# Kernel optimization log

Hardware: AMD Instinct MI355X
Metric: run time of the kernel (lower is better)

## Reference

```python
import jax, jax.numpy as jnp
import numpy as np

K = 1.0            # curvature (manifold.k); sqrt(K)=1 simplifies formulas
EPS = 1e-5         # module eps used in variance rescale
MIN_NORM = 1e-8    # clamp for sqrt of Lorentz inners
MAX_EUCLID = 10.0  # rescale_to_max_euclid cap (keeps cosh/sinh in fp32 range)


def l_inner(x, y):
    # Lorentz inner product <x,y>_L = -x0*y0 + <x_s, y_s>, keepdim
    return -x[..., :1] * y[..., :1] + jnp.sum(x[..., 1:] * y[..., 1:], axis=-1, keepdims=True)


def centroid(x):
    # Lorentzian centroid over the group axis (dim=-2)
    avg = jnp.mean(x, axis=-2, keepdims=True)
    denom = jnp.sqrt(jnp.clip(-l_inner(avg, avg), MIN_NORM, None))
    return avg / denom


def logmap(x, y):
    alpha = jnp.clip(-l_inner(x, y), 1.0 + 1e-7, None)   # -<x,y>_L >= 1
    dist = jnp.arccosh(alpha)
    nomin = y - alpha * x                                # y + <x,y>_L * x
    denom = jnp.sqrt(jnp.clip(l_inner(nomin, nomin), MIN_NORM, None))
    return dist * nomin / denom


def _plus_origin(p):
    # p + o where o = (1, 0, ..., 0)
    return jnp.concatenate([p[..., :1] + 1.0, p[..., 1:]], axis=-1)


def transp0back(x, v):
    # parallel transport of tangent v at x back to the origin o
    nom = -v[..., :1]                 # <o, v>_L = -v0
    denom = 1.0 + x[..., :1]          # K - <x, o>_L = 1 + x0
    return v + (nom / denom) * _plus_origin(x)


def transp0(y, v):
    # parallel transport of tangent v at origin o to point y
    nom = l_inner(y, v)
    denom = 1.0 + y[..., :1]          # K - <o, y>_L = 1 + y0
    return v + (nom / denom) * _plus_origin(y)


def rescale_to_max_euclid(u):
    n = jnp.linalg.norm(u, axis=-1, keepdims=True)
    scale = jnp.minimum(1.0, MAX_EUCLID / jnp.clip(n, MIN_NORM, None))
    return u * scale


def expmap(x, u):
    nrm = jnp.sqrt(jnp.clip(l_inner(u, u), MIN_NORM, None))
    return jnp.cosh(nrm) * x + jnp.sinh(nrm) * (u / nrm)


def setup_inputs() -> dict:
    key = jax.random.key(0)
    k1, = jax.random.split(key, 1)
    bs, h, w, c = 64, 56, 56, 128
    # sample spatial components, lift onto the hyperboloid: x0 = sqrt(1+|xs|^2)
    xs = 0.5 * jax.random.normal(k1, (bs, h, w, c - 1), dtype=jnp.float32)
    x0 = jnp.sqrt(1.0 + jnp.sum(xs * xs, axis=-1, keepdims=True))
    x = jnp.concatenate([x0, xs], axis=-1)
    gamma = jnp.ones((c,), dtype=jnp.float32)
    # beta = manifold.origin(c) = (1, 0, ..., 0)
    beta = jnp.zeros((c,), dtype=jnp.float32).at[0].set(1.0)
    return {"x": x, "gamma": gamma, "beta": beta, "groups": 8}


def reference(x, gamma, beta, groups):
    bs, h, w, c = x.shape
    xg = x.reshape(bs, -1, groups, c)                    # (bs, hw/g, g, c)
    mean = centroid(xg)                                  # (bs, hw/g, 1, c)
    x_T = logmap(mean, xg)                               # tangent at mean
    x_T = transp0back(mean, x_T)                         # tangent at origin
    # Frechet-style variance: mean Euclidean norm over spatial dim (dim=1)
    var = jnp.mean(jnp.linalg.norm(x_T, axis=-1, keepdims=True), axis=1, keepdims=True)
    x_T = x_T * (gamma / (var + EPS))
    x_T = rescale_to_max_euclid(x_T)
    x_T = transp0(beta, x_T)                             # transport to beta
    out = expmap(beta, x_T)
    return out.reshape(bs, h, w, c)
```

## Files before the change

### kernel.cpp

```cpp
#include <hip/hip_runtime.h>
#include <math.h>


constexpr int S_GROUPS = 392;
constexpr int N_GROUPS = 64 * S_GROUPS;
constexpr int CSTRIDE = 192;

__device__ __forceinline__ void wave_lds_fence() {
  __asm__ volatile("" ::: "memory");
  __builtin_amdgcn_wave_barrier();
  __asm__ volatile("" ::: "memory");
}

__device__ __forceinline__ void fold_mean(const float v[16], int lane,
                                          float& c0, float& c1) {
  float a8[8];
  const bool h5 = (lane & 32) != 0;
#pragma unroll
  for (int i = 0; i < 8; ++i) {
    float kp = h5 ? v[i + 8] : v[i];
    float sd = h5 ? v[i] : v[i + 8];
    a8[i] = kp + __shfl_xor(sd, 32, 64);
  }
  float a4[4];
  const bool h4 = (lane & 16) != 0;
#pragma unroll
  for (int i = 0; i < 4; ++i) {
    float kp = h4 ? a8[i + 4] : a8[i];
    float sd = h4 ? a8[i] : a8[i + 4];
    a4[i] = kp + __shfl_xor(sd, 16, 64);
  }
  const bool h3 = (lane & 8) != 0;
  float kp0 = h3 ? a4[2] : a4[0], sd0 = h3 ? a4[0] : a4[2];
  float kp1 = h3 ? a4[3] : a4[1], sd1 = h3 ? a4[1] : a4[3];
  c0 = (kp0 + __shfl_xor(sd0, 8, 64)) * 0.125f;
  c1 = (kp1 + __shfl_xor(sd1, 8, 64)) * 0.125f;
}

__global__ __launch_bounds__(256) void lngn_pass1(
    const float* __restrict__ x, const float* __restrict__ gamma,
    const float* __restrict__ beta, float* __restrict__ var_part,
    float* __restrict__ cache) {
  __shared__ float sm[4][128];
  const int w = threadIdx.x >> 6, lane = threadIdx.x & 63;
  const int p = lane >> 3, q = lane & 7;
  const int wid = blockIdx.x * 4 + w;
  const float* b0 = x + (size_t)wid * 1024 + p * 128 + q * 16;
  float* gc = cache + (size_t)wid * CSTRIDE;

  float v[16], gm[16], bt[16];
#pragma unroll
  for (int j = 0; j < 4; ++j) {
    *reinterpret_cast<float4*>(&v[4 * j]) =
        *reinterpret_cast<const float4*>(b0 + 4 * j);
    *reinterpret_cast<float4*>(&gm[4 * j]) =
        *reinterpret_cast<const float4*>(gamma + q * 16 + 4 * j);
    *reinterpret_cast<float4*>(&bt[4 * j]) =
        *reinterpret_cast<const float4*>(beta + q * 16 + 4 * j);
  }

  float c0, c1;
  fold_mean(v, lane, c0, c1);
  *reinterpret_cast<float2*>(&sm[w][q * 16 + p * 2]) = make_float2(c0, c1);
  wave_lds_fence();
  float avg[16];
#pragma unroll
  for (int j = 0; j < 4; ++j)
    *reinterpret_cast<float4*>(&avg[4 * j]) =
        *reinterpret_cast<const float4*>(&sm[w][q * 16 + 4 * j]);
  const float2 t2 = *reinterpret_cast<const float2*>(&sm[w][2 * lane]);
  *reinterpret_cast<float2*>(gc + 2 * lane) = t2;

  float pa = 0.f, pd = 0.f, py = 0.f;
  float Gyy = 0.f, Gya = 0.f, Gaa = 0.f, By = 0.f, Ba = 0.f;
#pragma unroll
  for (int i = 0; i < 16; ++i) {
    const float gy = gm[i] * v[i], ga = gm[i] * avg[i];
    pa = fmaf(avg[i], avg[i], pa);
    pd = fmaf(avg[i], v[i], pd);
    py = fmaf(v[i], v[i], py);
    Gyy = fmaf(gy, gy, Gyy);
    Gya = fmaf(gy, ga, Gya);
    Gaa = fmaf(ga, ga, Gaa);
    By = fmaf(bt[i], gy, By);
    Ba = fmaf(bt[i], ga, Ba);
  }
#pragma unroll
  for (int m = 1; m <= 4; m <<= 1) {
    pa += __shfl_xor(pa, m, 64);
    pd += __shfl_xor(pd, m, 64);
    py += __shfl_xor(py, m, 64);
    Gyy += __shfl_xor(Gyy, m, 64);
    Gya += __shfl_xor(Gya, m, 64);
    Gaa += __shfl_xor(Gaa, m, 64);
    By += __shfl_xor(By, m, 64);
    Ba += __shfl_xor(Ba, m, 64);
  }
  const float y0 = __shfl(v[0], lane & 56, 64);
  const float avg0 = __shfl(avg[0], 0, 64);
  const float gm0 = gamma[0], b0g0 = beta[0] * gamma[0];

  const float aaL = pa - 2.f * avg0 * avg0;
  const float rden = rsqrtf(fmaxf(-aaL, 1e-8f));
  const float mean0 = rden * avg0;
  const float yaL = pd - 2.f * avg0 * y0;
  const float yyL = py - 2.f * y0 * y0;
  const float a_raw = -yaL * rden;
  const float alpha = fmaxf(a_raw, 1.f + 1e-7f);
  const float t = alpha - 1.f;
  const float dist = log1pf(t + sqrtf(t * (alpha + 1.f)));
  const float inn = fmaxf(yyL + 2.f * alpha * a_raw - alpha * alpha, 1e-8f);
  const float sc = dist * rsqrtf(inn);
  const float am = alpha * rden;
  const float v0 = sc * (y0 - am * avg0);
  const float coef = -v0 / (1.f + mean0);
  const float k = coef * rden - sc * am;
  const float T0 = fmaf(sc, y0, k * avg0);
  const float na = sc * sc * py + k * k * pa + 2.f * sc * k * pd +
                   coef * coef + 2.f * coef * T0;
  const float nvar = sqrtf(fmaxf(na, 0.f));
  const float pe = sc * sc * Gyy + k * k * Gaa + 2.f * sc * k * Gya +
                   gm0 * gm0 * coef * (coef + 2.f * T0);
  const float pb = fmaf(sc, By, k * Ba) - b0g0 * (2.f * T0 + coef);
  const float XT0 = T0 + coef;

  if (q == 0) {
    *reinterpret_cast<float4*>(gc + 128 + p * 8) = make_float4(sc, k, coef, pe);
    *reinterpret_cast<float4*>(gc + 128 + p * 8 + 4) =
        make_float4(pb, XT0, 0.f, 0.f);
    const int b = wid / S_GROUPS;
    const int s = wid - b * S_GROUPS;
    var_part[(size_t)(b * 8 + p) * S_GROUPS + s] = nvar;
  }
}

__global__ __launch_bounds__(256) void lngn_finalize(
    const float* __restrict__ var_part, const float* __restrict__ beta,
    float* __restrict__ var_out) {
  const int wv = (int)((blockIdx.x * 256 + threadIdx.x) >> 6);
  const int lane = threadIdx.x & 63;
  const float* base = var_part + (size_t)wv * S_GROUPS;
  float s = 0.f;
  for (int s0 = lane; s0 < S_GROUPS; s0 += 64) s += base[s0];
#pragma unroll
  for (int m = 32; m >= 1; m >>= 1) s += __shfl_xor(s, m, 64);
  if (lane == 0) var_out[wv] = s * (1.f / (float)S_GROUPS);

  if (blockIdx.x == 0 && threadIdx.x < 64) {
    const int l = threadIdx.x;
    float b0v = beta[2 * l], b1v = beta[2 * l + 1];
    float tsum = b0v * b0v + b1v * b1v;
    if (l == 0) tsum -= 2.f * b0v * b0v;
#pragma unroll
    for (int m = 32; m >= 1; m >>= 1) tsum += __shfl_xor(tsum, m, 64);
    if (l == 0) var_out[512] = tsum;
  }
}

__global__ __launch_bounds__(256) void lngn_pass2(
    const float* __restrict__ x, const float* __restrict__ gamma,
    const float* __restrict__ beta, const float* __restrict__ var,
    const float* __restrict__ cache, float* __restrict__ out) {
  const int w = threadIdx.x >> 6, lane = threadIdx.x & 63;
  const int wid = blockIdx.x * 4 + w;
  const float* xb = x + (size_t)wid * 1024;
  const float* gc = cache + (size_t)wid * CSTRIDE;
  const int cl = lane & 31;
  const int par = lane >> 5;

  float4 xv[4];
#pragma unroll
  for (int j = 0; j < 4; ++j)
    xv[j] = *reinterpret_cast<const float4*>(xb + j * 256 + 4 * lane);
  const float4 av = *reinterpret_cast<const float4*>(gc + 4 * cl);
  const float4 gm4 = *reinterpret_cast<const float4*>(gamma + 4 * cl);
  const float4 bt4 = *reinterpret_cast<const float4*>(beta + 4 * cl);

  const int pix = lane & 7;
  const float4 s0 = *reinterpret_cast<const float4*>(gc + 128 + pix * 8);
  const float4 s1v = *reinterpret_cast<const float4*>(gc + 128 + pix * 8 + 4);
  const float sc = s0.x, kk = s0.y, coef = s0.z, PE = s0.w;
  const float PB = s1v.x, XT0 = s1v.y;
  const int b = wid / S_GROUPS;
  const float varv = var[b * 8 + pix];
  const float pbb = var[512];
  const float bt0 = beta[0], gm0 = gamma[0];

  const float is1 = 1.f / (varv + 1e-5f);
  const float pe = is1 * is1 * PE;
  const float pb = is1 * PB;
  const float u0 = is1 * gm0 * XT0;
  const float n = sqrtf(pe);
  const float scl = fminf(1.f, 10.f / fmaxf(n, 1e-8f));
  const float c2 = scl * pb / (1.f + bt0);
  const float uuL = pe - 2.f * u0 * u0;
  const float innw = scl * scl * uuL + 2.f * scl * c2 * (pb - u0) +
                     c2 * c2 * (pbb - 2.f * bt0 - 1.f);
  const float nrm = sqrtf(fmaxf(innw, 1e-8f));
  const float e = expf(nrm), ie = 1.f / e;
  const float chv = 0.5f * (e + ie);
  const float isn = (0.5f * (e - ie)) / nrm;
  const float A1 = chv + isn * c2;
  const float Cu = isn * scl * is1;
  const float A2 = Cu * sc;
  const float A3 = Cu * kk;
  const float A4 = fmaf(Cu * gm0, coef, isn * c2);

  float* ob = out + (size_t)wid * 1024;
#pragma unroll
  for (int j = 0; j < 4; ++j) {
    const int sp = 2 * j + par;
    const float a1 = __shfl(A1, sp, 64);
    const float a2 = __shfl(A2, sp, 64);
    const float a3 = __shfl(A3, sp, 64);
    const float a4 = __shfl(A4, sp, 64);
    float4 o4;
    o4.x = fmaf(a1, bt4.x, gm4.x * fmaf(a2, xv[j].x, a3 * av.x));
    o4.y = fmaf(a1, bt4.y, gm4.y * fmaf(a2, xv[j].y, a3 * av.y));
    o4.z = fmaf(a1, bt4.z, gm4.z * fmaf(a2, xv[j].z, a3 * av.z));
    o4.w = fmaf(a1, bt4.w, gm4.w * fmaf(a2, xv[j].w, a3 * av.w));
    if (cl == 0) o4.x += a4;
    *reinterpret_cast<float4*>(ob + j * 256 + 4 * lane) = o4;
  }
}

extern "C" void kernel_launch(void* const* d_in, const int* in_sizes, int n_in,
                              void* d_out, int out_size, void* d_ws,
                              size_t ws_size, hipStream_t stream) {
  const float* x = (const float*)d_in[0];
  const float* gamma = (const float*)d_in[1];
  const float* beta = (const float*)d_in[2];
  float* out = (float*)d_out;
  float* var_part = (float*)d_ws;
  float* var_final = var_part + (size_t)N_GROUPS * 8;
  float* cache = var_part + 201472;

  lngn_pass1<<<N_GROUPS / 4, 256, 0, stream>>>(x, gamma, beta, var_part, cache);
  lngn_finalize<<<128, 256, 0, stream>>>(var_part, beta, var_final);
  lngn_pass2<<<N_GROUPS / 4, 256, 0, stream>>>(x, gamma, beta, var_final, cache,
                                               out);
}
```

Baseline: 206.6 us.

## Use persistent grid-stride loops with next-group prefetch and DPP reductions

Both passes switch from one wave per group to a fixed 2048-block grid where each wave loops over groups. Pass 1 software-prefetches the next group's x slice into registers while computing the current one. The 8-lane reductions and the xor-8 shuffle in fold_mean become DPP row operations instead of ds_bpermute-based shuffles. This aims to hide load latency and cut launch and shuffle overhead, at the cost of extra registers, fewer resident blocks, and an odd leftover expression in fold_mean.

```diff
diff --git a/kernel.cpp b/kernel.cpp
--- a/kernel.cpp
+++ b/kernel.cpp
@@ -5,6 +5,10 @@
 constexpr int S_GROUPS = 392;
 constexpr int N_GROUPS = 64 * S_GROUPS;
 constexpr int CSTRIDE = 192;
+constexpr int P1_BLOCKS = 2048;
+constexpr int P1_WAVES = P1_BLOCKS * 4;
+constexpr int P2_BLOCKS = 2048;
+constexpr int P2_WAVES = P2_BLOCKS * 4;
 
 __device__ __forceinline__ void wave_lds_fence() {
   __asm__ volatile("" ::: "memory");
@@ -12,6 +16,23 @@
   __asm__ volatile("" ::: "memory");
 }
 
+template <int CTRL>
+__device__ __forceinline__ float dpp_add(float x) {
+  int y = __builtin_amdgcn_update_dpp(0, __float_as_int(x), CTRL, 0xF, 0xF, true);
+  return x + __int_as_float(y);
+}
+template <int CTRL>
+__device__ __forceinline__ float dpp_mov(float x) {
+  return __int_as_float(
+      __builtin_amdgcn_update_dpp(0, __float_as_int(x), CTRL, 0xF, 0xF, true));
+}
+__device__ __forceinline__ float qsum(float x) {
+  x = dpp_add<0xB1>(x);
+  x = dpp_add<0x4E>(x);
+  x = dpp_add<0x141>(x);
+  return x;
+}
+
 __device__ __forceinline__ void fold_mean(const float v[16], int lane,
                                           float& c0, float& c1) {
   float a8[8];
@@ -26,111 +47,131 @@
   const bool h4 = (lane & 16) != 0;
 #pragma unroll
   for (int i = 0; i < 4; ++i) {
-    float kp = h4 ? a8[i + 4] : a8[i];
+    float kp = h4 ? a4[0] * 0.f + (h4 ? a8[i + 4] : a8[i]) : a8[i];
     float sd = h4 ? a8[i] : a8[i + 4];
+    kp = h4 ? a8[i + 4] : a8[i];
     a4[i] = kp + __shfl_xor(sd, 16, 64);
   }
   const bool h3 = (lane & 8) != 0;
   float kp0 = h3 ? a4[2] : a4[0], sd0 = h3 ? a4[0] : a4[2];
   float kp1 = h3 ? a4[3] : a4[1], sd1 = h3 ? a4[1] : a4[3];
-  c0 = (kp0 + __shfl_xor(sd0, 8, 64)) * 0.125f;
-  c1 = (kp1 + __shfl_xor(sd1, 8, 64)) * 0.125f;
-}
-
-__global__ __launch_bounds__(256) void lngn_pass1(
+  c0 = (kp0 + dpp_mov<0x128>(sd0)) * 0.125f;
+  c1 = (kp1 + dpp_mov<0x128>(sd1)) * 0.125f;
+}
+
+__global__ __launch_bounds__(256, 4) void lngn_pass1(
     const float* __restrict__ x, const float* __restrict__ gamma,
     const float* __restrict__ beta, float* __restrict__ var_part,
     float* __restrict__ cache) {
   __shared__ float sm[4][128];
   const int w = threadIdx.x >> 6, lane = threadIdx.x & 63;
   const int p = lane >> 3, q = lane & 7;
-  const int wid = blockIdx.x * 4 + w;
-  const float* b0 = x + (size_t)wid * 1024 + p * 128 + q * 16;
-  float* gc = cache + (size_t)wid * CSTRIDE;
-
-  float v[16], gm[16], bt[16];
+  const int wstart = blockIdx.x * 4 + w;
+
+  float gm[16], bt[16];
 #pragma unroll
   for (int j = 0; j < 4; ++j) {
-    *reinterpret_cast<float4*>(&v[4 * j]) =
-        *reinterpret_cast<const float4*>(b0 + 4 * j);
     *reinterpret_cast<float4*>(&gm[4 * j]) =
         *reinterpret_cast<const float4*>(gamma + q * 16 + 4 * j);
     *reinterpret_cast<float4*>(&bt[4 * j]) =
         *reinterpret_cast<const float4*>(beta + q * 16 + 4 * j);
   }
-
-  float c0, c1;
-  fold_mean(v, lane, c0, c1);
-  *reinterpret_cast<float2*>(&sm[w][q * 16 + p * 2]) = make_float2(c0, c1);
-  wave_lds_fence();
-  float avg[16];
-#pragma unroll
-  for (int j = 0; j < 4; ++j)
-    *reinterpret_cast<float4*>(&avg[4 * j]) =
-        *reinterpret_cast<const float4*>(&sm[w][q * 16 + 4 * j]);
-  const float2 t2 = *reinterpret_cast<const float2*>(&sm[w][2 * lane]);
-  *reinterpret_cast<float2*>(gc + 2 * lane) = t2;
-
-  float pa = 0.f, pd = 0.f, py = 0.f;
-  float Gyy = 0.f, Gya = 0.f, Gaa = 0.f, By = 0.f, Ba = 0.f;
-#pragma unroll
-  for (int i = 0; i < 16; ++i) {
-    const float gy = gm[i] * v[i], ga = gm[i] * avg[i];
-    pa = fmaf(avg[i], avg[i], pa);
-    pd = fmaf(avg[i], v[i], pd);
-    py = fmaf(v[i], v[i], py);
-    Gyy = fmaf(gy, gy, Gyy);
-    Gya = fmaf(gy, ga, Gya);
-    Gaa = fmaf(ga, ga, Gaa);
-    By = fmaf(bt[i], gy, By);
-    Ba = fmaf(bt[i], ga, Ba);
-  }
-#pragma unroll
-  for (int m = 1; m <= 4; m <<= 1) {
-    pa += __shfl_xor(pa, m, 64);
-    pd += __shfl_xor(pd, m, 64);
-    py += __shfl_xor(py, m, 64);
-    Gyy += __shfl_xor(Gyy, m, 64);
-    Gya += __shfl_xor(Gya, m, 64);
-    Gaa += __shfl_xor(Gaa, m, 64);
-    By += __shfl_xor(By, m, 64);
-    Ba += __shfl_xor(Ba, m, 64);
-  }
-  const float y0 = __shfl(v[0], lane & 56, 64);
-  const float avg0 = __shfl(avg[0], 0, 64);
   const float gm0 = gamma[0], b0g0 = beta[0] * gamma[0];
-
-  const float aaL = pa - 2.f * avg0 * avg0;
-  const float rden = rsqrtf(fmaxf(-aaL, 1e-8f));
-  const float mean0 = rden * avg0;
-  const float yaL = pd - 2.f * avg0 * y0;
-  const float yyL = py - 2.f * y0 * y0;
-  const float a_raw = -yaL * rden;
-  const float alpha = fmaxf(a_raw, 1.f + 1e-7f);
-  const float t = alpha - 1.f;
-  const float dist = log1pf(t + sqrtf(t * (alpha + 1.f)));
-  const float inn = fmaxf(yyL + 2.f * alpha * a_raw - alpha * alpha, 1e-8f);
-  const float sc = dist * rsqrtf(inn);
-  const float am = alpha * rden;
-  const float v0 = sc * (y0 - am * avg0);
-  const float coef = -v0 / (1.f + mean0);
-  const float k = coef * rden - sc * am;
-  const float T0 = fmaf(sc, y0, k * avg0);
-  const float na = sc * sc * py + k * k * pa + 2.f * sc * k * pd +
-                   coef * coef + 2.f * coef * T0;
-  const float nvar = sqrtf(fmaxf(na, 0.f));
-  const float pe = sc * sc * Gyy + k * k * Gaa + 2.f * sc * k * Gya +
-                   gm0 * gm0 * coef * (coef + 2.f * T0);
-  const float pb = fmaf(sc, By, k * Ba) - b0g0 * (2.f * T0 + coef);
-  const float XT0 = T0 + coef;
-
-  if (q == 0) {
-    *reinterpret_cast<float4*>(gc + 128 + p * 8) = make_float4(sc, k, coef, pe);
-    *reinterpret_cast<float4*>(gc + 128 + p * 8 + 4) =
-        make_float4(pb, XT0, 0.f, 0.f);
-    const int b = wid / S_GROUPS;
-    const int s = wid - b * S_GROUPS;
-    var_part[(size_t)(b * 8 + p) * S_GROUPS + s] = nvar;
+  const int laneoff = p * 128 + q * 16;
+
+  int wid = wstart;
+  float v[16];
+  {
+    const float* b0 = x + (size_t)wid * 1024 + laneoff;
+#pragma unroll
+    for (int j = 0; j < 4; ++j)
+      *reinterpret_cast<float4*>(&v[4 * j]) =
+          *reinterpret_cast<const float4*>(b0 + 4 * j);
+  }
+
+  while (wid < N_GROUPS) {
+    const int wnext = wid + P1_WAVES;
+    float vn[16];
+    if (wnext < N_GROUPS) {
+      const float* bn = x + (size_t)wnext * 1024 + laneoff;
+#pragma unroll
+      for (int j = 0; j < 4; ++j)
+        *reinterpret_cast<float4*>(&vn[4 * j]) =
+            *reinterpret_cast<const float4*>(bn + 4 * j);
+    }
+    float* gc = cache + (size_t)wid * CSTRIDE;
+
+    float c0, c1;
+    fold_mean(v, lane, c0, c1);
+    *reinterpret_cast<float2*>(&sm[w][q * 16 + p * 2]) = make_float2(c0, c1);
+    wave_lds_fence();
+    float avg[16];
+#pragma unroll
+    for (int j = 0; j < 4; ++j)
+      *reinterpret_cast<float4*>(&avg[4 * j]) =
+          *reinterpret_cast<const float4*>(&sm[w][q * 16 + 4 * j]);
+    const float2 t2 = *reinterpret_cast<const float2*>(&sm[w][2 * lane]);
+    *reinterpret_cast<float2*>(gc + 2 * lane) = t2;
+    wave_lds_fence();
+
+    float pa = 0.f, pd = 0.f, py = 0.f;
+    float Gyy = 0.f, Gya = 0.f, Gaa = 0.f, By = 0.f, Ba = 0.f;
+#pragma unroll
+    for (int i = 0; i < 16; ++i) {
+      const float gy = gm[i] * v[i], ga = gm[i] * avg[i];
+      pa = fmaf(avg[i], avg[i], pa);
+      pd = fmaf(avg[i], v[i], pd);
+      py = fmaf(v[i], v[i], py);
+      Gyy = fmaf(gy, gy, Gyy);
+      Gya = fmaf(gy, ga, Gya);
+      Gaa = fmaf(ga, ga, Gaa);
+      By = fmaf(bt[i], gy, By);
+      Ba = fmaf(bt[i], ga, Ba);
+    }
+    pa = qsum(pa);  pd = qsum(pd);  py = qsum(py);
+    Gyy = qsum(Gyy); Gya = qsum(Gya); Gaa = qsum(Gaa);
+    By = qsum(By);  Ba = qsum(Ba);
+
+    const float y0 = __shfl(v[0], lane & 56, 64);
+    const float avg0 = __shfl(avg[0], 0, 64);
+
+    const float aaL = pa - 2.f * avg0 * avg0;
+    const float rden = rsqrtf(fmaxf(-aaL, 1e-8f));
+    const float mean0 = rden * avg0;
+    const float yaL = pd - 2.f * avg0 * y0;
+    const float yyL = py - 2.f * y0 * y0;
+    const float a_raw = -yaL * rden;
+    const float alpha = fmaxf(a_raw, 1.f + 1e-7f);
+    const float t = alpha - 1.f;
+    const float dist = log1pf(t + sqrtf(t * (alpha + 1.f)));
+    const float inn = fmaxf(yyL + 2.f * alpha * a_raw - alpha * alpha, 1e-8f);
+    const float sc = dist * rsqrtf(inn);
+    const float am = alpha * rden;
+    const float v0 = sc * (y0 - am * avg0);
+    const float coef = -v0 / (1.f + mean0);
+    const float k = coef * rden - sc * am;
+    const float T0 = fmaf(sc, y0, k * avg0);
+    const float na = sc * sc * py + k * k * pa + 2.f * sc * k * pd +
+                     coef * coef + 2.f * coef * T0;
+    const float nvar = sqrtf(fmaxf(na, 0.f));
+    const float pe = sc * sc * Gyy + k * k * Gaa + 2.f * sc * k * Gya +
+                     gm0 * gm0 * coef * (coef + 2.f * T0);
+    const float pb = fmaf(sc, By, k * Ba) - b0g0 * (2.f * T0 + coef);
+    const float XT0 = T0 + coef;
+
+    if (q == 0) {
+      *reinterpret_cast<float4*>(gc + 128 + p * 8) =
+          make_float4(sc, k, coef, pe);
+      *reinterpret_cast<float4*>(gc + 128 + p * 8 + 4) =
+          make_float4(pb, XT0, 0.f, 0.f);
+      const int b = wid / S_GROUPS;
+      const int s = wid - b * S_GROUPS;
+      var_part[(size_t)(b * 8 + p) * S_GROUPS + s] = nvar;
+    }
+
+#pragma unroll
+    for (int i = 0; i < 16; ++i) v[i] = vn[i];
+    wid = wnext;
   }
 }
 
@@ -162,65 +203,68 @@
     const float* __restrict__ beta, const float* __restrict__ var,
     const float* __restrict__ cache, float* __restrict__ out) {
   const int w = threadIdx.x >> 6, lane = threadIdx.x & 63;
-  const int wid = blockIdx.x * 4 + w;
-  const float* xb = x + (size_t)wid * 1024;
-  const float* gc = cache + (size_t)wid * CSTRIDE;
+  const int wstart = blockIdx.x * 4 + w;
   const int cl = lane & 31;
   const int par = lane >> 5;
-
-  float4 xv[4];
-#pragma unroll
-  for (int j = 0; j < 4; ++j)
-    xv[j] = *reinterpret_cast<const float4*>(xb + j * 256 + 4 * lane);
-  const float4 av = *reinterpret_cast<const float4*>(gc + 4 * cl);
+  const int pix = lane & 7;
+
   const float4 gm4 = *reinterpret_cast<const float4*>(gamma + 4 * cl);
   const float4 bt4 = *reinterpret_cast<const float4*>(beta + 4 * cl);
-
-  const int pix = lane & 7;
-  const float4 s0 = *reinterpret_cast<const float4*>(gc + 128 + pix * 8);
-  const float4 s1v = *reinterpret_cast<const float4*>(gc + 128 + pix * 8 + 4);
-  const float sc = s0.x, kk = s0.y, coef = s0.z, PE = s0.w;
-  const float PB = s1v.x, XT0 = s1v.y;
-  const int b = wid / S_GROUPS;
-  const float varv = var[b * 8 + pix];
   const float pbb = var[512];
   const float bt0 = beta[0], gm0 = gamma[0];
 
-  const float is1 = 1.f / (varv + 1e-5f);
-  const float pe = is1 * is1 * PE;
-  const float pb = is1 * PB;
-  const float u0 = is1 * gm0 * XT0;
-  const float n = sqrtf(pe);
-  const float scl = fminf(1.f, 10.f / fmaxf(n, 1e-8f));
-  const float c2 = scl * pb / (1.f + bt0);
-  const float uuL = pe - 2.f * u0 * u0;
-  const float innw = scl * scl * uuL + 2.f * scl * c2 * (pb - u0) +
-                     c2 * c2 * (pbb - 2.f * bt0 - 1.f);
-  const float nrm = sqrtf(fmaxf(innw, 1e-8f));
-  const float e = expf(nrm), ie = 1.f / e;
-  const float chv = 0.5f * (e + ie);
-  const float isn = (0.5f * (e - ie)) / nrm;
-  const float A1 = chv + isn * c2;
-  const float Cu = isn * scl * is1;
-  const float A2 = Cu * sc;
-  const float A3 = Cu * kk;
-  const float A4 = fmaf(Cu * gm0, coef, isn * c2);
-
-  float* ob = out + (size_t)wid * 1024;
-#pragma unroll
-  for (int j = 0; j < 4; ++j) {
-    const int sp = 2 * j + par;
-    const float a1 = __shfl(A1, sp, 64);
-    const float a2 = __shfl(A2, sp, 64);
-    const float a3 = __shfl(A3, sp, 64);
-    const float a4 = __shfl(A4, sp, 64);
-    float4 o4;
-    o4.x = fmaf(a1, bt4.x, gm4.x * fmaf(a2, xv[j].x, a3 * av.x));
-    o4.y = fmaf(a1, bt4.y, gm4.y * fmaf(a2, xv[j].y, a3 * av.y));
-    o4.z = fmaf(a1, bt4.z, gm4.z * fmaf(a2, xv[j].z, a3 * av.z));
-    o4.w = fmaf(a1, bt4.w, gm4.w * fmaf(a2, xv[j].w, a3 * av.w));
-    if (cl == 0) o4.x += a4;
-    *reinterpret_cast<float4*>(ob + j * 256 + 4 * lane) = o4;
+  for (int wid = wstart; wid < N_GROUPS; wid += P2_WAVES) {
+    const float* xb = x + (size_t)wid * 1024;
+    const float* gc = cache + (size_t)wid * CSTRIDE;
+
+    float4 xv[4];
+#pragma unroll
+    for (int j = 0; j < 4; ++j)
+      xv[j] = *reinterpret_cast<const float4*>(xb + j * 256 + 4 * lane);
+    const float4 av = *reinterpret_cast<const float4*>(gc + 4 * cl);
+    const float4 s0 = *reinterpret_cast<const float4*>(gc + 128 + pix * 8);
+    const float4 s1v = *reinterpret_cast<const float4*>(gc + 128 + pix * 8 + 4);
+    const float sc = s0.x, kk = s0.y, coef = s0.z, PE = s0.w;
+    const float PB = s1v.x, XT0 = s1v.y;
+    const int b = wid / S_GROUPS;
+    const float varv = var[b * 8 + pix];
+
+    const float is1 = 1.f / (varv + 1e-5f);
+    const float pe = is1 * is1 * PE;
+    const float pb = is1 * PB;
+    const float u0 = is1 * gm0 * XT0;
+    const float n = sqrtf(pe);
+    const float scl = fminf(1.f, 10.f / fmaxf(n, 1e-8f));
+    const float c2 = scl * pb / (1.f + bt0);
+    const float uuL = pe - 2.f * u0 * u0;
+    const float innw = scl * scl * uuL + 2.f * scl * c2 * (pb - u0) +
+                       c2 * c2 * (pbb - 2.f * bt0 - 1.f);
+    const float nrm = sqrtf(fmaxf(innw, 1e-8f));
+    const float e = expf(nrm), ie = 1.f / e;
+    const float chv = 0.5f * (e + ie);
+    const float isn = (0.5f * (e - ie)) / nrm;
+    const float A1 = chv + isn * c2;
+    const float Cu = isn * scl * is1;
+    const float A2 = Cu * sc;
+    const float A3 = Cu * kk;
+    const float A4 = fmaf(Cu * gm0, coef, isn * c2);
+
+    float* ob = out + (size_t)wid * 1024;
+#pragma unroll
+    for (int j = 0; j < 4; ++j) {
+      const int sp = 2 * j + par;
+      const float a1 = __shfl(A1, sp, 64);
+      const float a2 = __shfl(A2, sp, 64);
+      const float a3 = __shfl(A3, sp, 64);
+      const float a4 = __shfl(A4, sp, 64);
+      float4 o4;
+      o4.x = fmaf(a1, bt4.x, gm4.x * fmaf(a2, xv[j].x, a3 * av.x));
+      o4.y = fmaf(a1, bt4.y, gm4.y * fmaf(a2, xv[j].y, a3 * av.y));
+      o4.z = fmaf(a1, bt4.z, gm4.z * fmaf(a2, xv[j].z, a3 * av.z));
+      o4.w = fmaf(a1, bt4.w, gm4.w * fmaf(a2, xv[j].w, a3 * av.w));
+      if (cl == 0) o4.x += a4;
+      *reinterpret_cast<float4*>(ob + j * 256 + 4 * lane) = o4;
+    }
   }
 }
 
@@ -235,8 +279,8 @@
   float* var_final = var_part + (size_t)N_GROUPS * 8;
   float* cache = var_part + 201472;
 
-  lngn_pass1<<<N_GROUPS / 4, 256, 0, stream>>>(x, gamma, beta, var_part, cache);
+  lngn_pass1<<<P1_BLOCKS, 256, 0, stream>>>(x, gamma, beta, var_part, cache);
   lngn_finalize<<<128, 256, 0, stream>>>(var_part, beta, var_final);
-  lngn_pass2<<<N_GROUPS / 4, 256, 0, stream>>>(x, gamma, beta, var_final, cache,
-                                               out);
-}
+  lngn_pass2<<<P2_BLOCKS, 256, 0, stream>>>(x, gamma, beta, var_final, cache,
+                                            out);
+}
```

Measured after the change: 210.1 us. Within noise of the previous version (+1.7%).

## Make pass1 persistent with double-buffered global-to-LDS prefetch

Applied to the files above, without the earlier changes.

Pass1 becomes a persistent grid of 1024 blocks, each wave looping over many groups. Each wave prefetches the next two groups' 4 KB tiles into per-wave LDS double buffers using direct global_load_lds, with manual vmcnt and lgkmcnt waits. The goal is to hide global load latency behind the per-group reductions and scalar math. The cost is more LDS per block, an occupancy cap from launch bounds, fragile hand-placed waitcnt ordering, and a redundant reload on the last iterations.

```diff
diff --git a/kernel.cpp b/kernel.cpp
--- a/kernel.cpp
+++ b/kernel.cpp
@@ -5,11 +5,19 @@
 constexpr int S_GROUPS = 392;
 constexpr int N_GROUPS = 64 * S_GROUPS;
 constexpr int CSTRIDE = 192;
+constexpr int P1_BLOCKS = 1024;
+constexpr int P1_WAVES = P1_BLOCKS * 4;
 
 __device__ __forceinline__ void wave_lds_fence() {
   __asm__ volatile("" ::: "memory");
   __builtin_amdgcn_wave_barrier();
   __asm__ volatile("" ::: "memory");
+}
+
+__device__ __forceinline__ void gload16(const float* g, float* l) {
+  __builtin_amdgcn_global_load_lds(
+      (const __attribute__((address_space(1))) void*)g,
+      (__attribute__((address_space(3))) void*)l, 16, 0, 0);
 }
 
 __device__ __forceinline__ void fold_mean(const float v[16], int lane,
@@ -37,100 +45,140 @@
   c1 = (kp1 + __shfl_xor(sd1, 8, 64)) * 0.125f;
 }
 
-__global__ __launch_bounds__(256) void lngn_pass1(
+__global__ __launch_bounds__(256, 4) void lngn_pass1(
     const float* __restrict__ x, const float* __restrict__ gamma,
     const float* __restrict__ beta, float* __restrict__ var_part,
     float* __restrict__ cache) {
+  __shared__ float xb[4][2][1024];
   __shared__ float sm[4][128];
   const int w = threadIdx.x >> 6, lane = threadIdx.x & 63;
   const int p = lane >> 3, q = lane & 7;
-  const int wid = blockIdx.x * 4 + w;
-  const float* b0 = x + (size_t)wid * 1024 + p * 128 + q * 16;
-  float* gc = cache + (size_t)wid * CSTRIDE;
-
-  float v[16], gm[16], bt[16];
+  const int loff = p * 128 + q * 16;
+
+  float gm[16], bt[16];
 #pragma unroll
   for (int j = 0; j < 4; ++j) {
-    *reinterpret_cast<float4*>(&v[4 * j]) =
-        *reinterpret_cast<const float4*>(b0 + 4 * j);
     *reinterpret_cast<float4*>(&gm[4 * j]) =
         *reinterpret_cast<const float4*>(gamma + q * 16 + 4 * j);
     *reinterpret_cast<float4*>(&bt[4 * j]) =
         *reinterpret_cast<const float4*>(beta + q * 16 + 4 * j);
   }
-
-  float c0, c1;
-  fold_mean(v, lane, c0, c1);
-  *reinterpret_cast<float2*>(&sm[w][q * 16 + p * 2]) = make_float2(c0, c1);
-  wave_lds_fence();
-  float avg[16];
-#pragma unroll
-  for (int j = 0; j < 4; ++j)
-    *reinterpret_cast<float4*>(&avg[4 * j]) =
-        *reinterpret_cast<const float4*>(&sm[w][q * 16 + 4 * j]);
-  const float2 t2 = *reinterpret_cast<const float2*>(&sm[w][2 * lane]);
-  *reinterpret_cast<float2*>(gc + 2 * lane) = t2;
-
-  float pa = 0.f, pd = 0.f, py = 0.f;
-  float Gyy = 0.f, Gya = 0.f, Gaa = 0.f, By = 0.f, Ba = 0.f;
-#pragma unroll
-  for (int i = 0; i < 16; ++i) {
-    const float gy = gm[i] * v[i], ga = gm[i] * avg[i];
-    pa = fmaf(avg[i], avg[i], pa);
-    pd = fmaf(avg[i], v[i], pd);
-    py = fmaf(v[i], v[i], py);
-    Gyy = fmaf(gy, gy, Gyy);
-    Gya = fmaf(gy, ga, Gya);
-    Gaa = fmaf(ga, ga, Gaa);
-    By = fmaf(bt[i], gy, By);
-    Ba = fmaf(bt[i], ga, Ba);
-  }
-#pragma unroll
-  for (int m = 1; m <= 4; m <<= 1) {
-    pa += __shfl_xor(pa, m, 64);
-    pd += __shfl_xor(pd, m, 64);
-    py += __shfl_xor(py, m, 64);
-    Gyy += __shfl_xor(Gyy, m, 64);
-    Gya += __shfl_xor(Gya, m, 64);
-    Gaa += __shfl_xor(Gaa, m, 64);
-    By += __shfl_xor(By, m, 64);
-    Ba += __shfl_xor(Ba, m, 64);
-  }
-  const float y0 = __shfl(v[0], lane & 56, 64);
-  const float avg0 = __shfl(avg[0], 0, 64);
   const float gm0 = gamma[0], b0g0 = beta[0] * gamma[0];
-
-  const float aaL = pa - 2.f * avg0 * avg0;
-  const float rden = rsqrtf(fmaxf(-aaL, 1e-8f));
-  const float mean0 = rden * avg0;
-  const float yaL = pd - 2.f * avg0 * y0;
-  const float yyL = py - 2.f * y0 * y0;
-  const float a_raw = -yaL * rden;
-  const float alpha = fmaxf(a_raw, 1.f + 1e-7f);
-  const float t = alpha - 1.f;
-  const float dist = log1pf(t + sqrtf(t * (alpha + 1.f)));
-  const float inn = fmaxf(yyL + 2.f * alpha * a_raw - alpha * alpha, 1e-8f);
-  const float sc = dist * rsqrtf(inn);
-  const float am = alpha * rden;
-  const float v0 = sc * (y0 - am * avg0);
-  const float coef = -v0 / (1.f + mean0);
-  const float k = coef * rden - sc * am;
-  const float T0 = fmaf(sc, y0, k * avg0);
-  const float na = sc * sc * py + k * k * pa + 2.f * sc * k * pd +
-                   coef * coef + 2.f * coef * T0;
-  const float nvar = sqrtf(fmaxf(na, 0.f));
-  const float pe = sc * sc * Gyy + k * k * Gaa + 2.f * sc * k * Gya +
-                   gm0 * gm0 * coef * (coef + 2.f * T0);
-  const float pb = fmaf(sc, By, k * Ba) - b0g0 * (2.f * T0 + coef);
-  const float XT0 = T0 + coef;
-
-  if (q == 0) {
-    *reinterpret_cast<float4*>(gc + 128 + p * 8) = make_float4(sc, k, coef, pe);
-    *reinterpret_cast<float4*>(gc + 128 + p * 8 + 4) =
-        make_float4(pb, XT0, 0.f, 0.f);
-    const int b = wid / S_GROUPS;
-    const int s = wid - b * S_GROUPS;
-    var_part[(size_t)(b * 8 + p) * S_GROUPS + s] = nvar;
+  __builtin_amdgcn_sched_barrier(0);
+
+  const int w0 = blockIdx.x * 4 + w;
+  {
+    const float* g0 = x + (size_t)w0 * 1024 + loff;
+    const float* g1 = x + (size_t)(w0 + P1_WAVES) * 1024 + loff;
+#pragma unroll
+    for (int j = 0; j < 4; ++j) gload16(g0 + 4 * j, &xb[w][0][j * 256]);
+#pragma unroll
+    for (int j = 0; j < 4; ++j) gload16(g1 + 4 * j, &xb[w][1][j * 256]);
+  }
+  asm volatile("s_waitcnt vmcnt(0)" ::: "memory");
+  __builtin_amdgcn_sched_barrier(0);
+
+  int cur = 0;
+  bool first = true;
+  for (int wid = w0; wid < N_GROUPS; wid += P1_WAVES) {
+    if (!first) {
+      asm volatile("s_waitcnt vmcnt(8)" ::: "memory");
+      __builtin_amdgcn_sched_barrier(0);
+    }
+    first = false;
+
+    float v[16];
+#pragma unroll
+    for (int j = 0; j < 4; ++j)
+      *reinterpret_cast<float4*>(&v[4 * j]) =
+          *reinterpret_cast<const float4*>(&xb[w][cur][j * 256 + 4 * lane]);
+    asm volatile("s_waitcnt lgkmcnt(0)" ::: "memory");
+    __builtin_amdgcn_sched_barrier(0);
+    {
+      const int wpre = wid + 2 * P1_WAVES;
+      const float* g =
+          x + (size_t)(wpre < N_GROUPS ? wpre : wid) * 1024 + loff;
+#pragma unroll
+      for (int j = 0; j < 4; ++j) gload16(g + 4 * j, &xb[w][cur][j * 256]);
+    }
+    __builtin_amdgcn_sched_barrier(0);
+    cur ^= 1;
+
+    float* gc = cache + (size_t)wid * CSTRIDE;
+    float c0, c1;
+    fold_mean(v, lane, c0, c1);
+    *reinterpret_cast<float2*>(&sm[w][q * 16 + p * 2]) = make_float2(c0, c1);
+    wave_lds_fence();
+    float avg[16];
+#pragma unroll
+    for (int j = 0; j < 4; ++j)
+      *reinterpret_cast<float4*>(&avg[4 * j]) =
+          *reinterpret_cast<const float4*>(&sm[w][q * 16 + 4 * j]);
+    const float2 t2 = *reinterpret_cast<const float2*>(&sm[w][2 * lane]);
+    *reinterpret_cast<float2*>(gc + 2 * lane) = t2;
+    wave_lds_fence();
+
+    float pa = 0.f, pd = 0.f, py = 0.f;
+    float Gyy = 0.f, Gya = 0.f, Gaa = 0.f, By = 0.f, Ba = 0.f;
+#pragma unroll
+    for (int i = 0; i < 16; ++i) {
+      const float gy = gm[i] * v[i], ga = gm[i] * avg[i];
+      pa = fmaf(avg[i], avg[i], pa);
+      pd = fmaf(avg[i], v[i], pd);
+      py = fmaf(v[i], v[i], py);
+      Gyy = fmaf(gy, gy, Gyy);
+      Gya = fmaf(gy, ga, Gya);
+      Gaa = fmaf(ga, ga, Gaa);
+      By = fmaf(bt[i], gy, By);
+      Ba = fmaf(bt[i], ga, Ba);
+    }
+#pragma unroll
+    for (int m = 1; m <= 4; m <<= 1) {
+      pa += __shfl_xor(pa, m, 64);
+      pd += __shfl_xor(pd, m, 64);
+      py += __shfl_xor(py, m, 64);
+      Gyy += __shfl_xor(Gyy, m, 64);
+      Gya += __shfl_xor(Gya, m, 64);
+      Gaa += __shfl_xor(Gaa, m, 64);
+      By += __shfl_xor(By, m, 64);
+      Ba += __shfl_xor(Ba, m, 64);
+    }
+    const float y0 = __shfl(v[0], lane & 56, 64);
+    const float avg0 = __shfl(avg[0], 0, 64);
+
+    const float aaL = pa - 2.f * avg0 * avg0;
+    const float rden = rsqrtf(fmaxf(-aaL, 1e-8f));
+    const float mean0 = rden * avg0;
+    const float yaL = pd - 2.f * avg0 * y0;
+    const float yyL = py - 2.f * y0 * y0;
+    const float a_raw = -yaL * rden;
+    const float alpha = fmaxf(a_raw, 1.f + 1e-7f);
+    const float t = alpha - 1.f;
+    const float dist = log1pf(t + sqrtf(t * (alpha + 1.f)));
+    const float inn = fmaxf(yyL + 2.f * alpha * a_raw - alpha * alpha, 1e-8f);
+    const float sc = dist * rsqrtf(inn);
+    const float am = alpha * rden;
+    const float v0 = sc * (y0 - am * avg0);
+    const float coef = -v0 / (1.f + mean0);
+    const float k = coef * rden - sc * am;
+    const float T0 = fmaf(sc, y0, k * avg0);
+    const float na = sc * sc * py + k * k * pa + 2.f * sc * k * pd +
+                     coef * coef + 2.f * coef * T0;
+    const float nvar = sqrtf(fmaxf(na, 0.f));
+    const float pe = sc * sc * Gyy + k * k * Gaa + 2.f * sc * k * Gya +
+                     gm0 * gm0 * coef * (coef + 2.f * T0);
+    const float pb = fmaf(sc, By, k * Ba) - b0g0 * (2.f * T0 + coef);
+    const float XT0 = T0 + coef;
+
+    if (q == 0) {
+      *reinterpret_cast<float4*>(gc + 128 + p * 8) =
+          make_float4(sc, k, coef, pe);
+      *reinterpret_cast<float4*>(gc + 128 + p * 8 + 4) =
+          make_float4(pb, XT0, 0.f, 0.f);
+      const int b = wid / S_GROUPS;
+      const int s = wid - b * S_GROUPS;
+      var_part[(size_t)(b * 8 + p) * S_GROUPS + s] = nvar;
+    }
   }
 }
 
@@ -235,7 +283,7 @@
   float* var_final = var_part + (size_t)N_GROUPS * 8;
   float* cache = var_part + 201472;
 
-  lngn_pass1<<<N_GROUPS / 4, 256, 0, stream>>>(x, gamma, beta, var_part, cache);
+  lngn_pass1<<<P1_BLOCKS, 256, 0, stream>>>(x, gamma, beta, var_part, cache);
   lngn_finalize<<<128, 256, 0, stream>>>(var_part, beta, var_final);
   lngn_pass2<<<N_GROUPS / 4, 256, 0, stream>>>(x, gamma, beta, var_final, cache,
                                                out);
```

New measurement: 214.2 us. 1.04x slower.
